# Performance work log

Hardware: AMD Instinct MI355X
Metric: run time of the kernel (lower is better)

The kernel has to match this reference:

```python
import jax, jax.numpy as jnp
import numpy as np

N = 100000          # nodes
E = 1600000         # edges (before self-loops)
F_IN = 512          # num_node_features
H1, C1 = 8, 8       # layer-1 heads, per-head channels
NUM_CLASSES = 40
NEG_SLOPE = 0.2     # PyG GATConv default


def setup_inputs() -> dict:
    key = jax.random.key(0)
    ks = jax.random.split(key, 10)
    x = jax.random.normal(ks[0], (N, F_IN), jnp.float32)
    edge_index = jax.random.randint(ks[1], (2, E), 0, N, dtype=jnp.int64)
    # Glorot-ish scaled params (matches PyG init scale qualitatively)
    W1 = jax.random.normal(ks[2], (F_IN, H1 * C1), jnp.float32) / np.sqrt(F_IN)
    a_src1 = jax.random.normal(ks[3], (H1, C1), jnp.float32) / np.sqrt(C1)
    a_dst1 = jax.random.normal(ks[4], (H1, C1), jnp.float32) / np.sqrt(C1)
    b1 = jnp.zeros((H1 * C1,), jnp.float32)
    W2 = jax.random.normal(ks[5], (H1 * C1, NUM_CLASSES), jnp.float32) / np.sqrt(H1 * C1)
    a_src2 = jax.random.normal(ks[6], (1, NUM_CLASSES), jnp.float32) / np.sqrt(NUM_CLASSES)
    a_dst2 = jax.random.normal(ks[7], (1, NUM_CLASSES), jnp.float32) / np.sqrt(NUM_CLASSES)
    b2 = jnp.zeros((NUM_CLASSES,), jnp.float32)
    return {"x": x, "edge_index": edge_index, "W1": W1, "a_src1": a_src1,
            "a_dst1": a_dst1, "b1": b1, "W2": W2, "a_src2": a_src2,
            "a_dst2": a_dst2, "b2": b2}


def gat_layer(x, src, dst, W, a_s, a_d, b, concat):
    """PyG GATConv (eval mode: dropout=0). src -> dst messages, softmax over dst."""
    heads, ch = a_s.shape
    n = x.shape[0]
    h = (x @ W).reshape(n, heads, ch)                      # [N,H,C]
    alpha_s = jnp.einsum('nhc,hc->nh', h, a_s)             # [N,H]
    alpha_d = jnp.einsum('nhc,hc->nh', h, a_d)
    e = jax.nn.leaky_relu(alpha_s[src] + alpha_d[dst], NEG_SLOPE)   # [E,H]
    # segment softmax over incoming edges of each dst node
    m = jax.ops.segment_max(e, dst, num_segments=n)        # [N,H]
    p = jnp.exp(e - m[dst])
    s = jax.ops.segment_sum(p, dst, num_segments=n)
    alpha = p / (s[dst] + 1e-16)                           # [E,H]
    out = jax.ops.segment_sum(h[src] * alpha[..., None], dst, num_segments=n)  # [N,H,C]
    out = out.reshape(n, heads * ch) if concat else out.mean(axis=1)
    return out + b


def reference(x, edge_index, W1, a_src1, a_dst1, b1, W2, a_src2, a_dst2, b2):
    n = x.shape[0]
    loops = jnp.arange(n, dtype=edge_index.dtype)
    src = jnp.concatenate([edge_index[0], loops])          # add self-loops (PyG default)
    dst = jnp.concatenate([edge_index[1], loops])
    h = gat_layer(x, src, dst, W1, a_src1, a_dst1, b1, concat=True)
    h = jax.nn.elu(h)
    out = gat_layer(h, src, dst, W2, a_src2, a_dst2, b2, concat=False)
    return jax.nn.log_softmax(out, axis=1)
```

## Files before the change

kernel.cpp:

```cpp
#include <hip/hip_runtime.h>
#include <hip/hip_bf16.h>
#include <hip/hip_fp16.h>

#define F_IN 512
#define HC1 64
#define NH1 8
#define NC 40
#define NEG_SLOPE 0.2f
#define SCAN_CHUNK 2048
#define RADIX_EPB 4096
#define MAXNB 512
#define BCAP 8192

typedef short bf16x8 __attribute__((ext_vector_type(8)));
typedef float f32x4 __attribute__((ext_vector_type(4)));

static __device__ __forceinline__ unsigned short f2b(float f) {
    __hip_bfloat16 h = __float2bfloat16(f);
    return *(unsigned short*)&h;
}
static __device__ __forceinline__ float b2f(unsigned short u) {
    union { unsigned int i; float f; } v;
    v.i = ((unsigned int)u) << 16;
    return v.f;
}
static __device__ __forceinline__ unsigned short f2h(float f) {
    __half h = __float2half(f);
    return *(unsigned short*)&h;
}

__global__ void detect_i64(const int* __restrict__ ei, int* __restrict__ flag, int n_check) {
    __shared__ int found;
    if (threadIdx.x == 0) found = 0;
    __syncthreads();
    for (int i = threadIdx.x; i < n_check; i += 256) {
        if (ei[2 * i + 1] != 0) atomicOr(&found, 1);
    }
    __syncthreads();
    if (threadIdx.x == 0) *flag = (found == 0) ? 1 : 0;
}

__global__ void prep(const float* __restrict__ W1, const float* __restrict__ W2,
                     const float* __restrict__ a_s2, const float* __restrict__ a_d2,
                     unsigned short* __restrict__ wst, float* __restrict__ ws2,
                     float* __restrict__ wd2) {
    int t = blockIdx.x * 256 + threadIdx.x;
    if (t < 4096) {
        int p  = t & 7;
        int n  = (t >> 3) & 63;
        int kb = t >> 9;
        int l  = p ^ (n & 7);
        int k0 = kb * 64 + l * 8;
        unsigned short v[8];
#pragma unroll
        for (int j = 0; j < 8; j++) v[j] = f2b(W1[(size_t)(k0 + j) * HC1 + n]);
        *(uint4*)(wst + ((size_t)(kb * 64 + n) * 64 + p * 8)) = *(uint4*)v;
    }
    if (blockIdx.x == 0 && threadIdx.x < HC1) {
        int c = threadIdx.x;
        float s = 0.f, d = 0.f;
#pragma unroll
        for (int j = 0; j < NC; j++) {
            float w = W2[c * NC + j];
            s += w * a_s2[j];
            d += w * a_d2[j];
        }
        ws2[c] = s;
        wd2[c] = d;
    }
}

__global__ __launch_bounds__(256) void scatter1(const int* __restrict__ ei, const int* __restrict__ flag,
                                                int* __restrict__ deg, int* __restrict__ bcnt,
                                                int2* __restrict__ bpairs, int E, int NB) {
    __shared__ int cnt[MAXNB];
    __shared__ int gb[MAXNB];
    int tid = threadIdx.x;
    for (int i = tid; i < NB; i += 256) cnt[i] = 0;
    __syncthreads();
    int f = *flag;
    int base = blockIdx.x * RADIX_EPB;
    int sv[16], dv[16], rv[16];
#pragma unroll
    for (int i = 0; i < 16; i++) {
        int e = base + i * 256 + tid;
        if (e < E) {
            int s, d;
            if (f) { s = ei[2 * e]; d = ei[2 * (E + e)]; }
            else   { s = ei[e];     d = ei[E + e]; }
            sv[i] = s; dv[i] = d;
            rv[i] = atomicAdd(&cnt[d >> 8], 1);
            atomicAdd(&deg[d], 1);
        }
    }
    __syncthreads();
    for (int i = tid; i < NB; i += 256) {
        int c = cnt[i];
        gb[i] = c ? atomicAdd(&bcnt[i], c) : 0;
    }
    __syncthreads();
#pragma unroll
    for (int i = 0; i < 16; i++) {
        int e = base + i * 256 + tid;
        if (e < E) {
            int pos = gb[dv[i] >> 8] + rv[i];
            if (pos < BCAP)
                bpairs[(size_t)(dv[i] >> 8) * BCAP + pos] = make_int2(sv[i], dv[i]);
        }
    }
}

__global__ __launch_bounds__(256) void scan1(const int* __restrict__ deg, int* __restrict__ rowptr,
                                             int* __restrict__ bsums, int n) {
    __shared__ int sbuf[256];
    int tid = threadIdx.x;
    int base = blockIdx.x * SCAN_CHUNK + tid * 8;
    int v[8];
#pragma unroll
    for (int j = 0; j < 8; j++) { int idx = base + j; v[j] = (idx < n) ? deg[idx] : 0; }
    int tsum = 0;
#pragma unroll
    for (int j = 0; j < 8; j++) tsum += v[j];
    sbuf[tid] = tsum;
    __syncthreads();
    for (int off = 1; off < 256; off <<= 1) {
        int t = (tid >= off) ? sbuf[tid - off] : 0;
        __syncthreads();
        sbuf[tid] += t;
        __syncthreads();
    }
    int run = sbuf[tid] - tsum;
#pragma unroll
    for (int j = 0; j < 8; j++) {
        run += v[j];
        int idx = base + j;
        if (idx < n) rowptr[1 + idx] = run;
    }
    if (tid == 255) bsums[blockIdx.x] = sbuf[255];
}

__global__ __launch_bounds__(256) void scan23(int* __restrict__ rowptr,
                                              const int* __restrict__ bsums, int n, int nb) {
    __shared__ int soff[64];
    int tid = threadIdx.x;
    if (tid < 64) {
        int lane = tid;
        int v = (lane < nb) ? bsums[lane] : 0;
        int orig = v;
        for (int off = 1; off < 64; off <<= 1) {
            int t = __shfl_up(v, (unsigned)off, 64);
            if (lane >= off) v += t;
        }
        soff[lane] = v - orig;
    }
    __syncthreads();
    int i = blockIdx.x * 256 + tid;
    if (i < n) {
        rowptr[1 + i] += soff[i >> 11];
        if (i == 0) rowptr[0] = 0;
    }
}

__global__ __launch_bounds__(256) void scatter2(const int2* __restrict__ bpairs,
                                                const int* __restrict__ bcnt,
                                                const int* __restrict__ rowptr,
                                                int* __restrict__ col, int Nn) {
    __shared__ int cur[256];
    int b = blockIdx.x;
    int node0 = b << 8;
    int tid = threadIdx.x;
    int nlast = min(node0 + 256, Nn);
    if (node0 + tid < nlast) cur[tid] = rowptr[node0 + tid];
    __syncthreads();
    int cnt = min(bcnt[b], BCAP);
    const int2* bp = bpairs + (size_t)b * BCAP;
    for (int j = tid; j < cnt; j += 256) {
        int2 pr = bp[j];
        int pos = atomicAdd(&cur[pr.y - node0], 1);
        col[pos] = pr.x;
    }
}

__global__ __launch_bounds__(256) void gemm1(const float* __restrict__ x,
                                             const unsigned short* __restrict__ wst,
                                             const float* __restrict__ a_s, const float* __restrict__ a_d,
                                             unsigned short* __restrict__ h1, float* __restrict__ as1,
                                             float* __restrict__ ad1, int Nn) {
    __shared__ __align__(16) unsigned short smem[8192];
    unsigned short* xs = smem;
    unsigned short* ws = smem + 4096;
    int tid = threadIdx.x;
    int m0 = blockIdx.x * 64;
    int w = tid >> 6, lane = tid & 63;
    int quad = lane >> 4, mr = lane & 15;
    f32x4 acc[4];
#pragma unroll
    for (int i = 0; i < 4; i++) acc[i] = (f32x4){0.f, 0.f, 0.f, 0.f};

    int srow = tid >> 2;
    int sseg = tid & 3;
    bool rok = (m0 + srow) < Nn;
    const float* xrow = x + (size_t)(m0 + srow) * F_IN + sseg * 16;
    int swzw = (srow & 7) << 4;
    int swzr = (mr & 7) << 4;

    for (int kb = 0; kb < 8; kb++) {
        float4 xv0, xv1, xv2, xv3;
        if (rok) {
            const float4* xp = (const float4*)(xrow + kb * 64);
            xv0 = xp[0]; xv1 = xp[1]; xv2 = xp[2]; xv3 = xp[3];
        } else {
            xv0 = xv1 = xv2 = xv3 = make_float4(0.f, 0.f, 0.f, 0.f);
        }
        const uint4* wp = (const uint4*)(wst + (size_t)kb * 4096);
        uint4 wv0 = wp[tid];
        uint4 wv1 = wp[tid + 256];
        __syncthreads();
        {
            unsigned short bx[16];
            bx[0]  = f2b(xv0.x); bx[1]  = f2b(xv0.y); bx[2]  = f2b(xv0.z); bx[3]  = f2b(xv0.w);
            bx[4]  = f2b(xv1.x); bx[5]  = f2b(xv1.y); bx[6]  = f2b(xv1.z); bx[7]  = f2b(xv1.w);
            bx[8]  = f2b(xv2.x); bx[9]  = f2b(xv2.y); bx[10] = f2b(xv2.z); bx[11] = f2b(xv2.w);
            bx[12] = f2b(xv3.x); bx[13] = f2b(xv3.y); bx[14] = f2b(xv3.z); bx[15] = f2b(xv3.w);
            unsigned short* xr = xs + srow * 64;
            *(uint4*)(xr + ((((sseg * 32)      ) ^ swzw) >> 1)) = *(uint4*)&bx[0];
            *(uint4*)(xr + ((((sseg * 32) + 16 ) ^ swzw) >> 1)) = *(uint4*)&bx[8];
            ((uint4*)ws)[tid]       = wv0;
            ((uint4*)ws)[tid + 256] = wv1;
        }
        __syncthreads();
#pragma unroll
        for (int ks = 0; ks < 2; ks++) {
            int kc = ks * 64 + quad * 16;
            int co = (kc ^ swzr) >> 1;
            bf16x8 a = *(const bf16x8*)(xs + (w * 16 + mr) * 64 + co);
#pragma unroll
            for (int nb = 0; nb < 4; nb++) {
                bf16x8 b = *(const bf16x8*)(ws + (nb * 16 + mr) * 64 + co);
                acc[nb] = __builtin_amdgcn_mfma_f32_16x16x32_bf16(a, b, acc[nb], 0, 0, 0);
            }
        }
    }
    __syncthreads();
    unsigned short (*hs)[72] = (unsigned short(*)[72])smem;
#pragma unroll
    for (int nb = 0; nb < 4; nb++)
#pragma unroll
        for (int r = 0; r < 4; r++)
            hs[w * 16 + quad * 4 + r][nb * 16 + mr] = f2b(acc[nb][r]);
    __syncthreads();
    {
        if (rok) {
            uint4 v0 = *(const uint4*)&hs[srow][sseg * 16];
            uint4 v1 = *(const uint4*)&hs[srow][sseg * 16 + 8];
            uint4* dst = (uint4*)(h1 + (size_t)(m0 + srow) * HC1 + sseg * 16);
            dst[0] = v0;
            dst[1] = v1;
        }
    }
    for (int i = tid; i < 512; i += 256) {
        int row = i >> 3, hh = i & 7;
        if (m0 + row < Nn) {
            float s = 0.f, d = 0.f;
#pragma unroll
            for (int c = 0; c < 8; c++) {
                float v = b2f(hs[row][hh * 8 + c]);
                s += v * a_s[hh * 8 + c];
                d += v * a_d[hh * 8 + c];
            }
            as1[(size_t)(m0 + row) * NH1 + hh] = s;
            ad1[(size_t)(m0 + row) * NH1 + hh] = d;
        }
    }
}

__device__ __forceinline__ float lrelu(float e) { return e > 0.f ? e : NEG_SLOPE * e; }

__global__ __launch_bounds__(256) void agg1(const unsigned short* __restrict__ h1,
                                            const float* __restrict__ as1,
                                            const float* __restrict__ ad1, const int* __restrict__ rowptr,
                                            const int* __restrict__ col, const float* __restrict__ b1,
                                            const float* __restrict__ ws2, const float* __restrict__ wd2,
                                            unsigned short* __restrict__ h2b, float* __restrict__ as2,
                                            float* __restrict__ ad2, int Nn) {
    __shared__ float pbuf[4][NH1 * 68];
    int w = threadIdx.x >> 6;
    int wave = (blockIdx.x * 256 + threadIdx.x) >> 6;
    int lane = threadIdx.x & 63;
    if (wave >= Nn) return;
    int d = wave;
    int jb = rowptr[d], je = rowptr[d + 1];
    int half = lane >> 5;
    int cl = lane & 31;
    int head = cl >> 2;
    const float4* as4 = (const float4*)as1;
    const float4* ad4 = (const float4*)ad1;

    float4 dd0 = ad4[d * 2], dd1 = ad4[d * 2 + 1];
    float adh[8] = {dd0.x, dd0.y, dd0.z, dd0.w, dd1.x, dd1.y, dd1.z, dd1.w};
    float4 sd0 = as4[d * 2], sd1 = as4[d * 2 + 1];
    float svh[8] = {sd0.x, sd0.y, sd0.z, sd0.w, sd1.x, sd1.y, sd1.z, sd1.w};
    float e0[8];
#pragma unroll
    for (int h = 0; h < NH1; h++) e0[h] = lrelu(svh[h] + adh[h]);

    float acc0, acc1, ss;
    {
        unsigned gv = *(const unsigned*)(h1 + (size_t)d * HC1 + 2 * cl);
        union { unsigned i; float f; } lo, hi;
        lo.i = gv << 16; hi.i = gv & 0xffff0000u;
        if (half == 0) { acc0 = lo.f; acc1 = hi.f; ss = 1.f; }
        else           { acc0 = 0.f;  acc1 = 0.f;  ss = 0.f; }
    }
    float* pb = pbuf[w];

    for (int c0 = jb; c0 < je; c0 += 64) {
        int nc = min(64, je - c0);
        int srcv = d;
        if (lane < nc) {
            unsigned u = (unsigned)col[c0 + lane];
            srcv = (u < (unsigned)Nn) ? (int)u : d;
            float4 a0 = as4[srcv * 2], a1 = as4[srcv * 2 + 1];
            float ev[8] = {a0.x, a0.y, a0.z, a0.w, a1.x, a1.y, a1.z, a1.w};
#pragma unroll
            for (int h = 0; h < NH1; h++)
                pb[h * 68 + lane] = __expf(lrelu(ev[h] + adh[h]) - e0[h]);
        } else {
#pragma unroll
            for (int h = 0; h < NH1; h++) pb[h * 68 + lane] = 0.f;
        }
        int ncp = (nc + 7) & ~7;
        for (int jj = 0; jj < ncp; jj += 8) {
#pragma unroll
            for (int u4 = 0; u4 < 4; u4++) {
                int idx = jj + 2 * u4 + half;
                int s = __shfl(srcv, idx, 64);
                float p = pb[head * 68 + idx];
                unsigned gv = *(const unsigned*)(h1 + (size_t)s * HC1 + 2 * cl);
                union { unsigned i; float f; } lo, hi;
                lo.i = gv << 16; hi.i = gv & 0xffff0000u;
                acc0 += p * lo.f;
                acc1 += p * hi.f;
                ss += p;
            }
        }
    }
    acc0 += __shfl_xor(acc0, 32, 64);
    acc1 += __shfl_xor(acc1, 32, 64);
    ss   += __shfl_xor(ss, 32, 64);
    float inv = 1.f / (ss + 1e-16f);
    float o0 = acc0 * inv + b1[2 * cl];
    float o1 = acc1 * inv + b1[2 * cl + 1];
    o0 = o0 > 0.f ? o0 : __expf(o0) - 1.0f;
    o1 = o1 > 0.f ? o1 : __expf(o1) - 1.0f;
    if (half == 0) {
        unsigned pk = (unsigned)f2h(o0) | ((unsigned)f2h(o1) << 16);
        *(unsigned*)(h2b + (size_t)d * HC1 + 2 * cl) = pk;
    }
    float va = o0 * ws2[2 * cl] + o1 * ws2[2 * cl + 1];
    float vd = o0 * wd2[2 * cl] + o1 * wd2[2 * cl + 1];
#pragma unroll
    for (int off = 16; off; off >>= 1) {
        va += __shfl_xor(va, off, 64);
        vd += __shfl_xor(vd, off, 64);
    }
    if (lane == 0) { as2[d] = va; ad2[d] = vd; }
}

__global__ __launch_bounds__(256) void agg2(const unsigned short* __restrict__ h2b,
                                            const float* __restrict__ as2,
                                            const float* __restrict__ ad2, const int* __restrict__ rowptr,
                                            const int* __restrict__ col, const float* __restrict__ W2,
                                            const float* __restrict__ b2,
                                            float* __restrict__ out, int Nn) {
    __shared__ float pbuf[4][64];
    __shared__ float smv[4][64];
    __shared__ float W2s[HC1 * NC];
    int tid = threadIdx.x;
    for (int i = tid; i < HC1 * NC; i += 256) W2s[i] = W2[i];
    __syncthreads();
    int w = tid >> 6;
    int wave = (blockIdx.x * 256 + tid) >> 6;
    int lane = tid & 63;
    if (wave >= Nn) return;
    int d = wave;
    int jb = rowptr[d], je = rowptr[d + 1];
    int half = lane >> 5;
    int cl = lane & 31;
    float adv = ad2[d];
    float e0 = lrelu(as2[d] + adv);
    float acc0, acc1, ss;
    {
        unsigned gv = *(const unsigned*)(h2b + (size_t)d * HC1 + 2 * cl);
        union { unsigned u; __half2 h; } cv; cv.u = gv;
        float2 ff = __half22float2(cv.h);
        if (half == 0) { acc0 = ff.x; acc1 = ff.y; ss = 1.f; }
        else           { acc0 = 0.f;  acc1 = 0.f;  ss = 0.f; }
    }
    float* pb = pbuf[w];

    for (int c0 = jb; c0 < je; c0 += 64) {
        int nc = min(64, je - c0);
        int srcv = d;
        if (lane < nc) {
            unsigned u = (unsigned)col[c0 + lane];
            srcv = (u < (unsigned)Nn) ? (int)u : d;
            pb[lane] = __expf(lrelu(as2[srcv] + adv) - e0);
        } else {
            pb[lane] = 0.f;
        }
        int ncp = (nc + 7) & ~7;
        for (int jj = 0; jj < ncp; jj += 8) {
#pragma unroll
            for (int u4 = 0; u4 < 4; u4++) {
                int idx = jj + 2 * u4 + half;
                int s = __shfl(srcv, idx, 64);
                float p = pb[idx];
                unsigned gv = *(const unsigned*)(h2b + (size_t)s * HC1 + 2 * cl);
                union { unsigned u; __half2 h; } cv; cv.u = gv;
                float2 ff = __half22float2(cv.h);
                acc0 += p * ff.x;
                acc1 += p * ff.y;
                ss += p;
            }
        }
    }
    acc0 += __shfl_xor(acc0, 32, 64);
    acc1 += __shfl_xor(acc1, 32, 64);
    ss   += __shfl_xor(ss, 32, 64);
    float inv = 1.f / (ss + 1e-16f);
    if (half == 0) {
        smv[w][2 * cl]     = acc0 * inv;
        smv[w][2 * cl + 1] = acc1 * inv;
    }
    float o = 0.f;
    if (lane < NC) {
        o = b2[lane];
        const float* sv = smv[w];
#pragma unroll
        for (int c = 0; c < HC1; c++) o += sv[c] * W2s[c * NC + lane];
    }
    float vm = (lane < NC) ? o : -1e30f;
#pragma unroll
    for (int off = 32; off; off >>= 1) vm = fmaxf(vm, __shfl_xor(vm, off, 64));
    float ex = (lane < NC) ? __expf(o - vm) : 0.f;
#pragma unroll
    for (int off = 32; off; off >>= 1) ex += __shfl_xor(ex, off, 64);
    float lsm = o - vm - __logf(ex);
    if (lane < NC) out[(size_t)d * NC + lane] = lsm;
}

extern "C" void kernel_launch(void* const* d_in, const int* in_sizes, int n_in,
                              void* d_out, int out_size, void* d_ws, size_t ws_size,
                              hipStream_t stream) {
    const float* x      = (const float*)d_in[0];
    const int*   ei     = (const int*)d_in[1];
    const float* W1     = (const float*)d_in[2];
    const float* a_src1 = (const float*)d_in[3];
    const float* a_dst1 = (const float*)d_in[4];
    const float* b1     = (const float*)d_in[5];
    const float* W2     = (const float*)d_in[6];
    const float* a_src2 = (const float*)d_in[7];
    const float* a_dst2 = (const float*)d_in[8];
    const float* b2     = (const float*)d_in[9];
    float* out = (float*)d_out;

    const int N = in_sizes[0] / F_IN;
    const int E = in_sizes[1] / 2;
    const int NB = (N + 255) >> 8;

    char* p = (char*)d_ws;
    auto alloc = [&](size_t bytes) -> void* {
        void* r = (void*)p;
        p += (bytes + 255) & ~(size_t)255;
        return r;
    };
    int* deg    = (int*)alloc((size_t)N * 4);
    int* bcnt   = (int*)alloc((size_t)MAXNB * 4);
    int* rowptr = (int*)alloc(((size_t)N + 1) * 4);
    int* bsums  = (int*)alloc(64 * 4);
    int* flag   = (int*)alloc(256);
    int2* bpairs = (int2*)alloc((size_t)NB * BCAP * 8);
    int* col    = (int*)alloc((size_t)E * 4);
    unsigned short* h1  = (unsigned short*)alloc((size_t)N * HC1 * 2);
    float* as1  = (float*)alloc((size_t)N * NH1 * 4);
    float* ad1  = (float*)alloc((size_t)N * NH1 * 4);
    unsigned short* h2b = (unsigned short*)alloc((size_t)N * HC1 * 2);
    float* as2  = (float*)alloc((size_t)N * 4);
    float* ad2  = (float*)alloc((size_t)N * 4);
    unsigned short* wst = (unsigned short*)alloc(8 * 64 * 64 * 2);
    float* ws2  = (float*)alloc(HC1 * 4);
    float* wd2  = (float*)alloc(HC1 * 4);

    size_t zlen = (size_t)((char*)(bcnt + MAXNB) - (char*)deg);
    hipMemsetAsync(deg, 0, zlen, stream);
    detect_i64<<<1, 256, 0, stream>>>(ei, flag, 4096);
    prep<<<16, 256, 0, stream>>>(W1, W2, a_src2, a_dst2, wst, ws2, wd2);
    scatter1<<<(E + RADIX_EPB - 1) / RADIX_EPB, 256, 0, stream>>>(ei, flag, deg, bcnt, bpairs, E, NB);
    int nb = (N + SCAN_CHUNK - 1) / SCAN_CHUNK;
    scan1<<<nb, 256, 0, stream>>>(deg, rowptr, bsums, N);
    scan23<<<(N + 255) / 256, 256, 0, stream>>>(rowptr, bsums, N, nb);
    scatter2<<<NB, 256, 0, stream>>>(bpairs, bcnt, rowptr, col, N);

    gemm1<<<(N + 63) / 64, 256, 0, stream>>>(x, wst, a_src1, a_dst1, h1, as1, ad1, N);
    agg1<<<(N + 3) / 4, 256, 0, stream>>>(h1, as1, ad1, rowptr, col, b1, ws2, wd2, h2b, as2, ad2, N);

    agg2<<<(N + 3) / 4, 256, 0, stream>>>(h2b, as2, ad2, rowptr, col, W2, b2, out, N);
}
```

Measured before the change: 584.5 us.

## Widen per-lane gathers in GAT aggregation and fold int64 detection into prep

In agg1, each lane now gathers 4 bf16 channels (8-byte loads) and 4 neighbours are processed concurrently per wave instead of 2. In agg2, each lane gathers 8 fp16 channels (16-byte loads) and 8 neighbours run in parallel. The aim is fewer, wider memory transactions and more edges in flight per wave, paid for with extra cross-lane shuffle reductions and more accumulator registers. Separately, the int64 detection kernel is merged into prep as an extra block, removing one kernel launch.

```diff
diff --git a/kernel.cpp b/kernel.cpp
--- a/kernel.cpp
+++ b/kernel.cpp
@@ -29,23 +29,24 @@
     return *(unsigned short*)&h;
 }
 
-__global__ void detect_i64(const int* __restrict__ ei, int* __restrict__ flag, int n_check) {
-    __shared__ int found;
-    if (threadIdx.x == 0) found = 0;
-    __syncthreads();
-    for (int i = threadIdx.x; i < n_check; i += 256) {
-        if (ei[2 * i + 1] != 0) atomicOr(&found, 1);
-    }
-    __syncthreads();
-    if (threadIdx.x == 0) *flag = (found == 0) ? 1 : 0;
-}
-
 __global__ void prep(const float* __restrict__ W1, const float* __restrict__ W2,
                      const float* __restrict__ a_s2, const float* __restrict__ a_d2,
+                     const int* __restrict__ ei,
                      unsigned short* __restrict__ wst, float* __restrict__ ws2,
-                     float* __restrict__ wd2) {
+                     float* __restrict__ wd2, int* __restrict__ flag) {
+    if (blockIdx.x == 16) {
+        __shared__ int found;
+        if (threadIdx.x == 0) found = 0;
+        __syncthreads();
+        for (int i = threadIdx.x; i < 4096; i += 256) {
+            if (ei[2 * i + 1] != 0) atomicOr(&found, 1);
+        }
+        __syncthreads();
+        if (threadIdx.x == 0) *flag = (found == 0) ? 1 : 0;
+        return;
+    }
     int t = blockIdx.x * 256 + threadIdx.x;
-    if (t < 4096) {
+    {
         int p  = t & 7;
         int n  = (t >> 3) & 63;
         int kb = t >> 9;
@@ -290,9 +291,9 @@
     if (wave >= Nn) return;
     int d = wave;
     int jb = rowptr[d], je = rowptr[d + 1];
-    int half = lane >> 5;
-    int cl = lane & 31;
-    int head = cl >> 2;
+    int g = lane >> 4;
+    int cl = lane & 15;
+    int head = cl >> 1;
     const float4* as4 = (const float4*)as1;
     const float4* ad4 = (const float4*)ad1;
 
@@ -304,13 +305,13 @@
 #pragma unroll
     for (int h = 0; h < NH1; h++) e0[h] = lrelu(svh[h] + adh[h]);
 
-    float acc0, acc1, ss;
-    {
-        unsigned gv = *(const unsigned*)(h1 + (size_t)d * HC1 + 2 * cl);
-        union { unsigned i; float f; } lo, hi;
-        lo.i = gv << 16; hi.i = gv & 0xffff0000u;
-        if (half == 0) { acc0 = lo.f; acc1 = hi.f; ss = 1.f; }
-        else           { acc0 = 0.f;  acc1 = 0.f;  ss = 0.f; }
+    float a0 = 0.f, a1 = 0.f, a2 = 0.f, a3 = 0.f, ss = 0.f;
+    if (g == 0) {
+        uint2 gv = *(const uint2*)(h1 + (size_t)d * HC1 + 4 * cl);
+        union { unsigned i; float f; } t0, t1, t2, t3;
+        t0.i = gv.x << 16; t1.i = gv.x & 0xffff0000u;
+        t2.i = gv.y << 16; t3.i = gv.y & 0xffff0000u;
+        a0 = t0.f; a1 = t1.f; a2 = t2.f; a3 = t3.f; ss = 1.f;
     }
     float* pb = pbuf[w];
 
@@ -320,8 +321,8 @@
         if (lane < nc) {
             unsigned u = (unsigned)col[c0 + lane];
             srcv = (u < (unsigned)Nn) ? (int)u : d;
-            float4 a0 = as4[srcv * 2], a1 = as4[srcv * 2 + 1];
-            float ev[8] = {a0.x, a0.y, a0.z, a0.w, a1.x, a1.y, a1.z, a1.w};
+            float4 q0 = as4[srcv * 2], q1 = as4[srcv * 2 + 1];
+            float ev[8] = {q0.x, q0.y, q0.z, q0.w, q1.x, q1.y, q1.z, q1.w};
 #pragma unroll
             for (int h = 0; h < NH1; h++)
                 pb[h * 68 + lane] = __expf(lrelu(ev[h] + adh[h]) - e0[h]);
@@ -332,35 +333,50 @@
         int ncp = (nc + 7) & ~7;
         for (int jj = 0; jj < ncp; jj += 8) {
 #pragma unroll
-            for (int u4 = 0; u4 < 4; u4++) {
-                int idx = jj + 2 * u4 + half;
+            for (int u2 = 0; u2 < 2; u2++) {
+                int idx = jj + 4 * u2 + g;
                 int s = __shfl(srcv, idx, 64);
                 float p = pb[head * 68 + idx];
-                unsigned gv = *(const unsigned*)(h1 + (size_t)s * HC1 + 2 * cl);
-                union { unsigned i; float f; } lo, hi;
-                lo.i = gv << 16; hi.i = gv & 0xffff0000u;
-                acc0 += p * lo.f;
-                acc1 += p * hi.f;
+                uint2 gv = *(const uint2*)(h1 + (size_t)s * HC1 + 4 * cl);
+                union { unsigned i; float f; } t0, t1, t2, t3;
+                t0.i = gv.x << 16; t1.i = gv.x & 0xffff0000u;
+                t2.i = gv.y << 16; t3.i = gv.y & 0xffff0000u;
+                a0 += p * t0.f; a1 += p * t1.f;
+                a2 += p * t2.f; a3 += p * t3.f;
                 ss += p;
             }
         }
     }
-    acc0 += __shfl_xor(acc0, 32, 64);
-    acc1 += __shfl_xor(acc1, 32, 64);
-    ss   += __shfl_xor(ss, 32, 64);
+#pragma unroll
+    for (int off = 16; off <= 32; off <<= 1) {
+        a0 += __shfl_xor(a0, off, 64);
+        a1 += __shfl_xor(a1, off, 64);
+        a2 += __shfl_xor(a2, off, 64);
+        a3 += __shfl_xor(a3, off, 64);
+        ss += __shfl_xor(ss, off, 64);
+    }
     float inv = 1.f / (ss + 1e-16f);
-    float o0 = acc0 * inv + b1[2 * cl];
-    float o1 = acc1 * inv + b1[2 * cl + 1];
+    float4 bv = *(const float4*)(b1 + 4 * cl);
+    float o0 = a0 * inv + bv.x;
+    float o1 = a1 * inv + bv.y;
+    float o2 = a2 * inv + bv.z;
+    float o3 = a3 * inv + bv.w;
     o0 = o0 > 0.f ? o0 : __expf(o0) - 1.0f;
     o1 = o1 > 0.f ? o1 : __expf(o1) - 1.0f;
-    if (half == 0) {
-        unsigned pk = (unsigned)f2h(o0) | ((unsigned)f2h(o1) << 16);
-        *(unsigned*)(h2b + (size_t)d * HC1 + 2 * cl) = pk;
-    }
-    float va = o0 * ws2[2 * cl] + o1 * ws2[2 * cl + 1];
-    float vd = o0 * wd2[2 * cl] + o1 * wd2[2 * cl + 1];
-#pragma unroll
-    for (int off = 16; off; off >>= 1) {
+    o2 = o2 > 0.f ? o2 : __expf(o2) - 1.0f;
+    o3 = o3 > 0.f ? o3 : __expf(o3) - 1.0f;
+    if (g == 0) {
+        uint2 pk;
+        pk.x = (unsigned)f2h(o0) | ((unsigned)f2h(o1) << 16);
+        pk.y = (unsigned)f2h(o2) | ((unsigned)f2h(o3) << 16);
+        *(uint2*)(h2b + (size_t)d * HC1 + 4 * cl) = pk;
+    }
+    float4 wsv = *(const float4*)(ws2 + 4 * cl);
+    float4 wdv = *(const float4*)(wd2 + 4 * cl);
+    float va = o0 * wsv.x + o1 * wsv.y + o2 * wsv.z + o3 * wsv.w;
+    float vd = o0 * wdv.x + o1 * wdv.y + o2 * wdv.z + o3 * wdv.w;
+#pragma unroll
+    for (int off = 1; off <= 8; off <<= 1) {
         va += __shfl_xor(va, off, 64);
         vd += __shfl_xor(vd, off, 64);
     }
@@ -385,17 +401,24 @@
     if (wave >= Nn) return;
     int d = wave;
     int jb = rowptr[d], je = rowptr[d + 1];
-    int half = lane >> 5;
-    int cl = lane & 31;
+    int g = lane >> 3;
+    int cl = lane & 7;
     float adv = ad2[d];
     float e0 = lrelu(as2[d] + adv);
-    float acc0, acc1, ss;
-    {
-        unsigned gv = *(const unsigned*)(h2b + (size_t)d * HC1 + 2 * cl);
-        union { unsigned u; __half2 h; } cv; cv.u = gv;
-        float2 ff = __half22float2(cv.h);
-        if (half == 0) { acc0 = ff.x; acc1 = ff.y; ss = 1.f; }
-        else           { acc0 = 0.f;  acc1 = 0.f;  ss = 0.f; }
+    float ac[8];
+    float ss = 0.f;
+#pragma unroll
+    for (int i = 0; i < 8; i++) ac[i] = 0.f;
+    if (g == 0) {
+        uint4 gv = *(const uint4*)(h2b + (size_t)d * HC1 + 8 * cl);
+        const unsigned* gw = (const unsigned*)&gv;
+#pragma unroll
+        for (int j = 0; j < 4; j++) {
+            union { unsigned u; __half2 h; } cv; cv.u = gw[j];
+            float2 ff = __half22float2(cv.h);
+            ac[2 * j] = ff.x; ac[2 * j + 1] = ff.y;
+        }
+        ss = 1.f;
     }
     float* pb = pbuf[w];
 
@@ -409,29 +432,38 @@
         } else {
             pb[lane] = 0.f;
         }
-        int ncp = (nc + 7) & ~7;
-        for (int jj = 0; jj < ncp; jj += 8) {
-#pragma unroll
-            for (int u4 = 0; u4 < 4; u4++) {
-                int idx = jj + 2 * u4 + half;
+        int ncp = (nc + 15) & ~15;
+        for (int jj = 0; jj < ncp; jj += 16) {
+#pragma unroll
+            for (int u2 = 0; u2 < 2; u2++) {
+                int idx = jj + 8 * u2 + g;
                 int s = __shfl(srcv, idx, 64);
                 float p = pb[idx];
-                unsigned gv = *(const unsigned*)(h2b + (size_t)s * HC1 + 2 * cl);
-                union { unsigned u; __half2 h; } cv; cv.u = gv;
-                float2 ff = __half22float2(cv.h);
-                acc0 += p * ff.x;
-                acc1 += p * ff.y;
+                uint4 gv = *(const uint4*)(h2b + (size_t)s * HC1 + 8 * cl);
+                const unsigned* gw = (const unsigned*)&gv;
+#pragma unroll
+                for (int j = 0; j < 4; j++) {
+                    union { unsigned u; __half2 h; } cv; cv.u = gw[j];
+                    float2 ff = __half22float2(cv.h);
+                    ac[2 * j]     += p * ff.x;
+                    ac[2 * j + 1] += p * ff.y;
+                }
                 ss += p;
             }
         }
     }
-    acc0 += __shfl_xor(acc0, 32, 64);
-    acc1 += __shfl_xor(acc1, 32, 64);
-    ss   += __shfl_xor(ss, 32, 64);
+#pragma unroll
+    for (int off = 8; off <= 32; off <<= 1) {
+#pragma unroll
+        for (int i = 0; i < 8; i++) ac[i] += __shfl_xor(ac[i], off, 64);
+        ss += __shfl_xor(ss, off, 64);
+    }
     float inv = 1.f / (ss + 1e-16f);
-    if (half == 0) {
-        smv[w][2 * cl]     = acc0 * inv;
-        smv[w][2 * cl + 1] = acc1 * inv;
+    if (g == 0) {
+        float4 v0 = make_float4(ac[0] * inv, ac[1] * inv, ac[2] * inv, ac[3] * inv);
+        float4 v1 = make_float4(ac[4] * inv, ac[5] * inv, ac[6] * inv, ac[7] * inv);
+        *(float4*)&smv[w][8 * cl]     = v0;
+        *(float4*)&smv[w][8 * cl + 4] = v1;
     }
     float o = 0.f;
     if (lane < NC) {
@@ -494,8 +526,7 @@
 
     size_t zlen = (size_t)((char*)(bcnt + MAXNB) - (char*)deg);
     hipMemsetAsync(deg, 0, zlen, stream);
-    detect_i64<<<1, 256, 0, stream>>>(ei, flag, 4096);
-    prep<<<16, 256, 0, stream>>>(W1, W2, a_src2, a_dst2, wst, ws2, wd2);
+    prep<<<17, 256, 0, stream>>>(W1, W2, a_src2, a_dst2, ei, wst, ws2, wd2, flag);
     scatter1<<<(E + RADIX_EPB - 1) / RADIX_EPB, 256, 0, stream>>>(ei, flag, deg, bcnt, bpairs, E, NB);
     int nb = (N + SCAN_CHUNK - 1) / SCAN_CHUNK;
     scan1<<<nb, 256, 0, stream>>>(deg, rowptr, bsums, N);
```

After: 588.0 us. Within noise of the previous version (+0.6%).

## Replace CSR build with 64-node edge buckets and shared-memory atomic aggregation

Applied to the files above, without the earlier changes.

Drops the degree count, prefix scans and second scatter pass. Edges are bucketed by destination into blocks of 64 nodes, stored as packed (src<<6 | local dst) ints, and each block accumulates messages into LDS with atomics. The i64 detection is folded into the prep launch. This saves several launches and CSR passes, but it adds LDS atomic contention, silently drops edges when a bucket exceeds its fixed capacity, and relies on src fitting in 25 bits.

```diff
diff --git a/kernel.cpp b/kernel.cpp
--- a/kernel.cpp
+++ b/kernel.cpp
@@ -7,10 +7,9 @@
 #define NH1 8
 #define NC 40
 #define NEG_SLOPE 0.2f
-#define SCAN_CHUNK 2048
 #define RADIX_EPB 4096
-#define MAXNB 512
-#define BCAP 8192
+#define MAXNB2 2048
+#define BCAP2 2048
 
 typedef short bf16x8 __attribute__((ext_vector_type(8)));
 typedef float f32x4 __attribute__((ext_vector_type(4)));
@@ -29,23 +28,26 @@
     return *(unsigned short*)&h;
 }
 
-__global__ void detect_i64(const int* __restrict__ ei, int* __restrict__ flag, int n_check) {
-    __shared__ int found;
-    if (threadIdx.x == 0) found = 0;
-    __syncthreads();
-    for (int i = threadIdx.x; i < n_check; i += 256) {
-        if (ei[2 * i + 1] != 0) atomicOr(&found, 1);
-    }
-    __syncthreads();
-    if (threadIdx.x == 0) *flag = (found == 0) ? 1 : 0;
-}
+__device__ __forceinline__ float lrelu(float e) { return e > 0.f ? e : NEG_SLOPE * e; }
 
 __global__ void prep(const float* __restrict__ W1, const float* __restrict__ W2,
                      const float* __restrict__ a_s2, const float* __restrict__ a_d2,
+                     const int* __restrict__ ei,
                      unsigned short* __restrict__ wst, float* __restrict__ ws2,
-                     float* __restrict__ wd2) {
+                     float* __restrict__ wd2, int* __restrict__ flag) {
+    if (blockIdx.x == 16) {
+        __shared__ int found;
+        if (threadIdx.x == 0) found = 0;
+        __syncthreads();
+        for (int i = threadIdx.x; i < 4096; i += 256) {
+            if (ei[2 * i + 1] != 0) atomicOr(&found, 1);
+        }
+        __syncthreads();
+        if (threadIdx.x == 0) *flag = (found == 0) ? 1 : 0;
+        return;
+    }
     int t = blockIdx.x * 256 + threadIdx.x;
-    if (t < 4096) {
+    {
         int p  = t & 7;
         int n  = (t >> 3) & 63;
         int kb = t >> 9;
@@ -71,16 +73,16 @@
 }
 
 __global__ __launch_bounds__(256) void scatter1(const int* __restrict__ ei, const int* __restrict__ flag,
-                                                int* __restrict__ deg, int* __restrict__ bcnt,
-                                                int2* __restrict__ bpairs, int E, int NB) {
-    __shared__ int cnt[MAXNB];
-    __shared__ int gb[MAXNB];
+                                                int* __restrict__ bcnt, int* __restrict__ bpk,
+                                                int E, int NB2) {
+    __shared__ int cnt[MAXNB2];
+    __shared__ int gb[MAXNB2];
     int tid = threadIdx.x;
-    for (int i = tid; i < NB; i += 256) cnt[i] = 0;
+    for (int i = tid; i < NB2; i += 256) cnt[i] = 0;
     __syncthreads();
     int f = *flag;
     int base = blockIdx.x * RADIX_EPB;
-    int sv[16], dv[16], rv[16];
+    int pk[16], bk[16], rv[16];
 #pragma unroll
     for (int i = 0; i < 16; i++) {
         int e = base + i * 256 + tid;
@@ -88,13 +90,13 @@
             int s, d;
             if (f) { s = ei[2 * e]; d = ei[2 * (E + e)]; }
             else   { s = ei[e];     d = ei[E + e]; }
-            sv[i] = s; dv[i] = d;
-            rv[i] = atomicAdd(&cnt[d >> 8], 1);
-            atomicAdd(&deg[d], 1);
-        }
-    }
-    __syncthreads();
-    for (int i = tid; i < NB; i += 256) {
+            pk[i] = (s << 6) | (d & 63);
+            bk[i] = d >> 6;
+            rv[i] = atomicAdd(&cnt[bk[i]], 1);
+        }
+    }
+    __syncthreads();
+    for (int i = tid; i < NB2; i += 256) {
         int c = cnt[i];
         gb[i] = c ? atomicAdd(&bcnt[i], c) : 0;
     }
@@ -103,81 +105,10 @@
     for (int i = 0; i < 16; i++) {
         int e = base + i * 256 + tid;
         if (e < E) {
-            int pos = gb[dv[i] >> 8] + rv[i];
-            if (pos < BCAP)
-                bpairs[(size_t)(dv[i] >> 8) * BCAP + pos] = make_int2(sv[i], dv[i]);
-        }
-    }
-}
-
-__global__ __launch_bounds__(256) void scan1(const int* __restrict__ deg, int* __restrict__ rowptr,
-                                             int* __restrict__ bsums, int n) {
-    __shared__ int sbuf[256];
-    int tid = threadIdx.x;
-    int base = blockIdx.x * SCAN_CHUNK + tid * 8;
-    int v[8];
-#pragma unroll
-    for (int j = 0; j < 8; j++) { int idx = base + j; v[j] = (idx < n) ? deg[idx] : 0; }
-    int tsum = 0;
-#pragma unroll
-    for (int j = 0; j < 8; j++) tsum += v[j];
-    sbuf[tid] = tsum;
-    __syncthreads();
-    for (int off = 1; off < 256; off <<= 1) {
-        int t = (tid >= off) ? sbuf[tid - off] : 0;
-        __syncthreads();
-        sbuf[tid] += t;
-        __syncthreads();
-    }
-    int run = sbuf[tid] - tsum;
-#pragma unroll
-    for (int j = 0; j < 8; j++) {
-        run += v[j];
-        int idx = base + j;
-        if (idx < n) rowptr[1 + idx] = run;
-    }
-    if (tid == 255) bsums[blockIdx.x] = sbuf[255];
-}
-
-__global__ __launch_bounds__(256) void scan23(int* __restrict__ rowptr,
-                                              const int* __restrict__ bsums, int n, int nb) {
-    __shared__ int soff[64];
-    int tid = threadIdx.x;
-    if (tid < 64) {
-        int lane = tid;
-        int v = (lane < nb) ? bsums[lane] : 0;
-        int orig = v;
-        for (int off = 1; off < 64; off <<= 1) {
-            int t = __shfl_up(v, (unsigned)off, 64);
-            if (lane >= off) v += t;
-        }
-        soff[lane] = v - orig;
-    }
-    __syncthreads();
-    int i = blockIdx.x * 256 + tid;
-    if (i < n) {
-        rowptr[1 + i] += soff[i >> 11];
-        if (i == 0) rowptr[0] = 0;
-    }
-}
-
-__global__ __launch_bounds__(256) void scatter2(const int2* __restrict__ bpairs,
-                                                const int* __restrict__ bcnt,
-                                                const int* __restrict__ rowptr,
-                                                int* __restrict__ col, int Nn) {
-    __shared__ int cur[256];
-    int b = blockIdx.x;
-    int node0 = b << 8;
-    int tid = threadIdx.x;
-    int nlast = min(node0 + 256, Nn);
-    if (node0 + tid < nlast) cur[tid] = rowptr[node0 + tid];
-    __syncthreads();
-    int cnt = min(bcnt[b], BCAP);
-    const int2* bp = bpairs + (size_t)b * BCAP;
-    for (int j = tid; j < cnt; j += 256) {
-        int2 pr = bp[j];
-        int pos = atomicAdd(&cur[pr.y - node0], 1);
-        col[pos] = pr.x;
+            int pos = gb[bk[i]] + rv[i];
+            if (pos < BCAP2)
+                bpk[(size_t)bk[i] * BCAP2 + pos] = pk[i];
+        }
     }
 }
 
@@ -274,180 +205,217 @@
     }
 }
 
-__device__ __forceinline__ float lrelu(float e) { return e > 0.f ? e : NEG_SLOPE * e; }
-
-__global__ __launch_bounds__(256) void agg1(const unsigned short* __restrict__ h1,
-                                            const float* __restrict__ as1,
-                                            const float* __restrict__ ad1, const int* __restrict__ rowptr,
-                                            const int* __restrict__ col, const float* __restrict__ b1,
-                                            const float* __restrict__ ws2, const float* __restrict__ wd2,
-                                            unsigned short* __restrict__ h2b, float* __restrict__ as2,
-                                            float* __restrict__ ad2, int Nn) {
-    __shared__ float pbuf[4][NH1 * 68];
-    int w = threadIdx.x >> 6;
-    int wave = (blockIdx.x * 256 + threadIdx.x) >> 6;
-    int lane = threadIdx.x & 63;
-    if (wave >= Nn) return;
-    int d = wave;
-    int jb = rowptr[d], je = rowptr[d + 1];
-    int half = lane >> 5;
-    int cl = lane & 31;
-    int head = cl >> 2;
-    const float4* as4 = (const float4*)as1;
-    const float4* ad4 = (const float4*)ad1;
-
-    float4 dd0 = ad4[d * 2], dd1 = ad4[d * 2 + 1];
-    float adh[8] = {dd0.x, dd0.y, dd0.z, dd0.w, dd1.x, dd1.y, dd1.z, dd1.w};
-    float4 sd0 = as4[d * 2], sd1 = as4[d * 2 + 1];
-    float svh[8] = {sd0.x, sd0.y, sd0.z, sd0.w, sd1.x, sd1.y, sd1.z, sd1.w};
-    float e0[8];
-#pragma unroll
-    for (int h = 0; h < NH1; h++) e0[h] = lrelu(svh[h] + adh[h]);
-
-    float acc0, acc1, ss;
+__global__ __launch_bounds__(256) void agg1b(const unsigned short* __restrict__ h1,
+                                             const float* __restrict__ as1,
+                                             const float* __restrict__ ad1,
+                                             const int* __restrict__ bcnt, const int* __restrict__ bpk,
+                                             const float* __restrict__ b1,
+                                             const float* __restrict__ ws2, const float* __restrict__ wd2,
+                                             unsigned short* __restrict__ h2b, float* __restrict__ as2,
+                                             float* __restrict__ ad2, int Nn) {
+    __shared__ float acc[64][68];
+    __shared__ float psum1[64][8];
+    __shared__ float ad1s[64][8];
+    __shared__ float e0s[64][8];
+    int tid = threadIdx.x;
+    int b = blockIdx.x;
+    int node0 = b << 6;
     {
-        unsigned gv = *(const unsigned*)(h1 + (size_t)d * HC1 + 2 * cl);
-        union { unsigned i; float f; } lo, hi;
-        lo.i = gv << 16; hi.i = gv & 0xffff0000u;
-        if (half == 0) { acc0 = lo.f; acc1 = hi.f; ss = 1.f; }
-        else           { acc0 = 0.f;  acc1 = 0.f;  ss = 0.f; }
-    }
-    float* pb = pbuf[w];
-
-    for (int c0 = jb; c0 < je; c0 += 64) {
-        int nc = min(64, je - c0);
-        int srcv = d;
-        if (lane < nc) {
-            unsigned u = (unsigned)col[c0 + lane];
-            srcv = (u < (unsigned)Nn) ? (int)u : d;
-            float4 a0 = as4[srcv * 2], a1 = as4[srcv * 2 + 1];
-            float ev[8] = {a0.x, a0.y, a0.z, a0.w, a1.x, a1.y, a1.z, a1.w};
-#pragma unroll
-            for (int h = 0; h < NH1; h++)
-                pb[h * 68 + lane] = __expf(lrelu(ev[h] + adh[h]) - e0[h]);
-        } else {
-#pragma unroll
-            for (int h = 0; h < NH1; h++) pb[h * 68 + lane] = 0.f;
-        }
-        int ncp = (nc + 7) & ~7;
-        for (int jj = 0; jj < ncp; jj += 8) {
-#pragma unroll
-            for (int u4 = 0; u4 < 4; u4++) {
-                int idx = jj + 2 * u4 + half;
-                int s = __shfl(srcv, idx, 64);
-                float p = pb[head * 68 + idx];
-                unsigned gv = *(const unsigned*)(h1 + (size_t)s * HC1 + 2 * cl);
-                union { unsigned i; float f; } lo, hi;
-                lo.i = gv << 16; hi.i = gv & 0xffff0000u;
-                acc0 += p * lo.f;
-                acc1 += p * hi.f;
-                ss += p;
-            }
-        }
-    }
-    acc0 += __shfl_xor(acc0, 32, 64);
-    acc1 += __shfl_xor(acc1, 32, 64);
-    ss   += __shfl_xor(ss, 32, 64);
-    float inv = 1.f / (ss + 1e-16f);
-    float o0 = acc0 * inv + b1[2 * cl];
-    float o1 = acc1 * inv + b1[2 * cl + 1];
-    o0 = o0 > 0.f ? o0 : __expf(o0) - 1.0f;
-    o1 = o1 > 0.f ? o1 : __expf(o1) - 1.0f;
-    if (half == 0) {
-        unsigned pk = (unsigned)f2h(o0) | ((unsigned)f2h(o1) << 16);
-        *(unsigned*)(h2b + (size_t)d * HC1 + 2 * cl) = pk;
-    }
-    float va = o0 * ws2[2 * cl] + o1 * ws2[2 * cl + 1];
-    float vd = o0 * wd2[2 * cl] + o1 * wd2[2 * cl + 1];
-#pragma unroll
-    for (int off = 16; off; off >>= 1) {
-        va += __shfl_xor(va, off, 64);
-        vd += __shfl_xor(vd, off, 64);
-    }
-    if (lane == 0) { as2[d] = va; ad2[d] = vd; }
-}
-
-__global__ __launch_bounds__(256) void agg2(const unsigned short* __restrict__ h2b,
-                                            const float* __restrict__ as2,
-                                            const float* __restrict__ ad2, const int* __restrict__ rowptr,
-                                            const int* __restrict__ col, const float* __restrict__ W2,
-                                            const float* __restrict__ b2,
-                                            float* __restrict__ out, int Nn) {
-    __shared__ float pbuf[4][64];
-    __shared__ float smv[4][64];
+        int n = tid >> 3, seg = tid & 7;
+#pragma unroll
+        for (int pass = 0; pass < 2; pass++) {
+            int nn = pass * 32 + n;
+            int gn = node0 + nn;
+            uint4 hv = make_uint4(0, 0, 0, 0);
+            if (gn < Nn) hv = *(const uint4*)(h1 + (size_t)gn * HC1 + seg * 8);
+            const unsigned* hw = (const unsigned*)&hv;
+#pragma unroll
+            for (int j = 0; j < 4; j++) {
+                acc[nn][seg * 8 + 2 * j]     = b2f((unsigned short)(hw[j] & 0xffff));
+                acc[nn][seg * 8 + 2 * j + 1] = b2f((unsigned short)(hw[j] >> 16));
+            }
+        }
+    }
+    for (int i = tid; i < 512; i += 256) {
+        int n = i >> 3, h = i & 7;
+        int gn = node0 + n;
+        float adv = 0.f, asv = 0.f;
+        if (gn < Nn) { adv = ad1[(size_t)gn * 8 + h]; asv = as1[(size_t)gn * 8 + h]; }
+        ad1s[n][h] = adv;
+        e0s[n][h] = lrelu(asv + adv);
+        psum1[n][h] = 1.f;
+    }
+    __syncthreads();
+    int cb = min(bcnt[b], BCAP2);
+    const int* bp = bpk + (size_t)b * BCAP2;
+    int w = tid >> 6, lane = tid & 63;
+    int g = lane >> 3, cl = lane & 7;
+    for (int eb = w * 16; eb < cb; eb += 64) {
+        int eA = eb + g, eB = eb + 8 + g;
+        int pkA = (eA < cb) ? bp[eA] : -1;
+        int pkB = (eB < cb) ? bp[eB] : -1;
+        if (pkA >= 0) {
+            int src = pkA >> 6, dl = pkA & 63;
+            float p = __expf(lrelu(as1[(size_t)src * 8 + cl] + ad1s[dl][cl]) - e0s[dl][cl]);
+            uint4 hv = *(const uint4*)(h1 + (size_t)src * HC1 + cl * 8);
+            const unsigned* hw = (const unsigned*)&hv;
+#pragma unroll
+            for (int j = 0; j < 4; j++) {
+                atomicAdd(&acc[dl][cl * 8 + 2 * j],     p * b2f((unsigned short)(hw[j] & 0xffff)));
+                atomicAdd(&acc[dl][cl * 8 + 2 * j + 1], p * b2f((unsigned short)(hw[j] >> 16)));
+            }
+            atomicAdd(&psum1[dl][cl], p);
+        }
+        if (pkB >= 0) {
+            int src = pkB >> 6, dl = pkB & 63;
+            float p = __expf(lrelu(as1[(size_t)src * 8 + cl] + ad1s[dl][cl]) - e0s[dl][cl]);
+            uint4 hv = *(const uint4*)(h1 + (size_t)src * HC1 + cl * 8);
+            const unsigned* hw = (const unsigned*)&hv;
+#pragma unroll
+            for (int j = 0; j < 4; j++) {
+                atomicAdd(&acc[dl][cl * 8 + 2 * j],     p * b2f((unsigned short)(hw[j] & 0xffff)));
+                atomicAdd(&acc[dl][cl * 8 + 2 * j + 1], p * b2f((unsigned short)(hw[j] >> 16)));
+            }
+            atomicAdd(&psum1[dl][cl], p);
+        }
+    }
+    __syncthreads();
+    {
+        int nloc = tid >> 5;
+        int c2 = (tid & 31) * 2;
+        int hh = c2 >> 3;
+        float2 bv = *(const float2*)(b1 + c2);
+        float2 wsv = *(const float2*)(ws2 + c2);
+        float2 wdv = *(const float2*)(wd2 + c2);
+#pragma unroll
+        for (int pass = 0; pass < 8; pass++) {
+            int n = pass * 8 + nloc;
+            int gn = node0 + n;
+            if (gn < Nn) {
+                float inv = 1.f / (psum1[n][hh] + 1e-16f);
+                float o0 = acc[n][c2] * inv + bv.x;
+                float o1 = acc[n][c2 + 1] * inv + bv.y;
+                o0 = o0 > 0.f ? o0 : __expf(o0) - 1.0f;
+                o1 = o1 > 0.f ? o1 : __expf(o1) - 1.0f;
+                unsigned pk = (unsigned)f2h(o0) | ((unsigned)f2h(o1) << 16);
+                *(unsigned*)(h2b + (size_t)gn * HC1 + c2) = pk;
+                float va = o0 * wsv.x + o1 * wsv.y;
+                float vd = o0 * wdv.x + o1 * wdv.y;
+#pragma unroll
+                for (int off = 1; off <= 16; off <<= 1) {
+                    va += __shfl_xor(va, off, 64);
+                    vd += __shfl_xor(vd, off, 64);
+                }
+                if ((tid & 31) == 0) { as2[gn] = va; ad2[gn] = vd; }
+            }
+        }
+    }
+}
+
+__global__ __launch_bounds__(256) void agg2b(const unsigned short* __restrict__ h2b,
+                                             const float* __restrict__ as2,
+                                             const float* __restrict__ ad2,
+                                             const int* __restrict__ bcnt, const int* __restrict__ bpk,
+                                             const float* __restrict__ W2, const float* __restrict__ b2,
+                                             float* __restrict__ out, int Nn) {
+    __shared__ float acc[64][68];
+    __shared__ float psum[64];
+    __shared__ float e0v[64], adv[64];
     __shared__ float W2s[HC1 * NC];
     int tid = threadIdx.x;
+    int b = blockIdx.x;
+    int node0 = b << 6;
     for (int i = tid; i < HC1 * NC; i += 256) W2s[i] = W2[i];
-    __syncthreads();
-    int w = tid >> 6;
-    int wave = (blockIdx.x * 256 + tid) >> 6;
-    int lane = tid & 63;
-    if (wave >= Nn) return;
-    int d = wave;
-    int jb = rowptr[d], je = rowptr[d + 1];
-    int half = lane >> 5;
-    int cl = lane & 31;
-    float adv = ad2[d];
-    float e0 = lrelu(as2[d] + adv);
-    float acc0, acc1, ss;
     {
-        unsigned gv = *(const unsigned*)(h2b + (size_t)d * HC1 + 2 * cl);
-        union { unsigned u; __half2 h; } cv; cv.u = gv;
-        float2 ff = __half22float2(cv.h);
-        if (half == 0) { acc0 = ff.x; acc1 = ff.y; ss = 1.f; }
-        else           { acc0 = 0.f;  acc1 = 0.f;  ss = 0.f; }
-    }
-    float* pb = pbuf[w];
-
-    for (int c0 = jb; c0 < je; c0 += 64) {
-        int nc = min(64, je - c0);
-        int srcv = d;
-        if (lane < nc) {
-            unsigned u = (unsigned)col[c0 + lane];
-            srcv = (u < (unsigned)Nn) ? (int)u : d;
-            pb[lane] = __expf(lrelu(as2[srcv] + adv) - e0);
-        } else {
-            pb[lane] = 0.f;
-        }
-        int ncp = (nc + 7) & ~7;
-        for (int jj = 0; jj < ncp; jj += 8) {
-#pragma unroll
-            for (int u4 = 0; u4 < 4; u4++) {
-                int idx = jj + 2 * u4 + half;
-                int s = __shfl(srcv, idx, 64);
-                float p = pb[idx];
-                unsigned gv = *(const unsigned*)(h2b + (size_t)s * HC1 + 2 * cl);
-                union { unsigned u; __half2 h; } cv; cv.u = gv;
+        int n = tid >> 3, seg = tid & 7;
+#pragma unroll
+        for (int pass = 0; pass < 2; pass++) {
+            int nn = pass * 32 + n;
+            int gn = node0 + nn;
+            uint4 hv = make_uint4(0, 0, 0, 0);
+            if (gn < Nn) hv = *(const uint4*)(h2b + (size_t)gn * HC1 + seg * 8);
+            const unsigned* hw = (const unsigned*)&hv;
+#pragma unroll
+            for (int j = 0; j < 4; j++) {
+                union { unsigned u; __half2 h; } cv; cv.u = hw[j];
                 float2 ff = __half22float2(cv.h);
-                acc0 += p * ff.x;
-                acc1 += p * ff.y;
-                ss += p;
-            }
-        }
-    }
-    acc0 += __shfl_xor(acc0, 32, 64);
-    acc1 += __shfl_xor(acc1, 32, 64);
-    ss   += __shfl_xor(ss, 32, 64);
-    float inv = 1.f / (ss + 1e-16f);
-    if (half == 0) {
-        smv[w][2 * cl]     = acc0 * inv;
-        smv[w][2 * cl + 1] = acc1 * inv;
-    }
-    float o = 0.f;
-    if (lane < NC) {
-        o = b2[lane];
-        const float* sv = smv[w];
-#pragma unroll
-        for (int c = 0; c < HC1; c++) o += sv[c] * W2s[c * NC + lane];
-    }
-    float vm = (lane < NC) ? o : -1e30f;
-#pragma unroll
-    for (int off = 32; off; off >>= 1) vm = fmaxf(vm, __shfl_xor(vm, off, 64));
-    float ex = (lane < NC) ? __expf(o - vm) : 0.f;
-#pragma unroll
-    for (int off = 32; off; off >>= 1) ex += __shfl_xor(ex, off, 64);
-    float lsm = o - vm - __logf(ex);
-    if (lane < NC) out[(size_t)d * NC + lane] = lsm;
+                acc[nn][seg * 8 + 2 * j]     = ff.x;
+                acc[nn][seg * 8 + 2 * j + 1] = ff.y;
+            }
+        }
+        if (tid < 64) {
+            psum[tid] = 1.f;
+            int gn = node0 + tid;
+            float a = 0.f, s = 0.f;
+            if (gn < Nn) { a = ad2[gn]; s = as2[gn]; }
+            adv[tid] = a;
+            e0v[tid] = lrelu(s + a);
+        }
+    }
+    __syncthreads();
+    int cb = min(bcnt[b], BCAP2);
+    const int* bp = bpk + (size_t)b * BCAP2;
+    int w = tid >> 6, lane = tid & 63;
+    int g = lane >> 3, cl = lane & 7;
+    for (int eb = w * 16; eb < cb; eb += 64) {
+        int eA = eb + g, eB = eb + 8 + g;
+        int pkA = (eA < cb) ? bp[eA] : -1;
+        int pkB = (eB < cb) ? bp[eB] : -1;
+        if (pkA >= 0) {
+            int src = pkA >> 6, dl = pkA & 63;
+            float p = __expf(lrelu(as2[src] + adv[dl]) - e0v[dl]);
+            uint4 hv = *(const uint4*)(h2b + (size_t)src * HC1 + cl * 8);
+            const unsigned* hw = (const unsigned*)&hv;
+#pragma unroll
+            for (int j = 0; j < 4; j++) {
+                union { unsigned u; __half2 h; } cv; cv.u = hw[j];
+                float2 ff = __half22float2(cv.h);
+                atomicAdd(&acc[dl][cl * 8 + 2 * j],     p * ff.x);
+                atomicAdd(&acc[dl][cl * 8 + 2 * j + 1], p * ff.y);
+            }
+            if (cl == 0) atomicAdd(&psum[dl], p);
+        }
+        if (pkB >= 0) {
+            int src = pkB >> 6, dl = pkB & 63;
+            float p = __expf(lrelu(as2[src] + adv[dl]) - e0v[dl]);
+            uint4 hv = *(const uint4*)(h2b + (size_t)src * HC1 + cl * 8);
+            const unsigned* hw = (const unsigned*)&hv;
+#pragma unroll
+            for (int j = 0; j < 4; j++) {
+                union { unsigned u; __half2 h; } cv; cv.u = hw[j];
+                float2 ff = __half22float2(cv.h);
+                atomicAdd(&acc[dl][cl * 8 + 2 * j],     p * ff.x);
+                atomicAdd(&acc[dl][cl * 8 + 2 * j + 1], p * ff.y);
+            }
+            if (cl == 0) atomicAdd(&psum[dl], p);
+        }
+    }
+    __syncthreads();
+    for (int i = 0; i < 16; i++) {
+        int n = w * 16 + i;
+        int gn = node0 + n;
+        if (gn >= Nn) break;
+        float inv = 1.f / (psum[n] + 1e-16f);
+        float o = 0.f;
+        if (lane < NC) {
+            float dot = 0.f;
+#pragma unroll
+            for (int c = 0; c < HC1; c += 4) {
+                float4 av = *(const float4*)&acc[n][c];
+                dot += av.x * W2s[(c + 0) * NC + lane] + av.y * W2s[(c + 1) * NC + lane]
+                     + av.z * W2s[(c + 2) * NC + lane] + av.w * W2s[(c + 3) * NC + lane];
+            }
+            o = b2[lane] + inv * dot;
+        }
+        float vm = (lane < NC) ? o : -1e30f;
+#pragma unroll
+        for (int off = 32; off; off >>= 1) vm = fmaxf(vm, __shfl_xor(vm, off, 64));
+        float ex = (lane < NC) ? __expf(o - vm) : 0.f;
+#pragma unroll
+        for (int off = 32; off; off >>= 1) ex += __shfl_xor(ex, off, 64);
+        float lsm = o - vm - __logf(ex);
+        if (lane < NC) out[(size_t)gn * NC + lane] = lsm;
+    }
 }
 
 extern "C" void kernel_launch(void* const* d_in, const int* in_sizes, int n_in,
@@ -467,7 +435,7 @@
 
     const int N = in_sizes[0] / F_IN;
     const int E = in_sizes[1] / 2;
-    const int NB = (N + 255) >> 8;
+    const int NB2 = (N + 63) >> 6;
 
     char* p = (char*)d_ws;
     auto alloc = [&](size_t bytes) -> void* {
@@ -475,13 +443,9 @@
         p += (bytes + 255) & ~(size_t)255;
         return r;
     };
-    int* deg    = (int*)alloc((size_t)N * 4);
-    int* bcnt   = (int*)alloc((size_t)MAXNB * 4);
-    int* rowptr = (int*)alloc(((size_t)N + 1) * 4);
-    int* bsums  = (int*)alloc(64 * 4);
+    int* bcnt   = (int*)alloc((size_t)NB2 * 4);
     int* flag   = (int*)alloc(256);
-    int2* bpairs = (int2*)alloc((size_t)NB * BCAP * 8);
-    int* col    = (int*)alloc((size_t)E * 4);
+    int* bpk    = (int*)alloc((size_t)NB2 * BCAP2 * 4);
     unsigned short* h1  = (unsigned short*)alloc((size_t)N * HC1 * 2);
     float* as1  = (float*)alloc((size_t)N * NH1 * 4);
     float* ad1  = (float*)alloc((size_t)N * NH1 * 4);
@@ -492,18 +456,12 @@
     float* ws2  = (float*)alloc(HC1 * 4);
     float* wd2  = (float*)alloc(HC1 * 4);
 
-    size_t zlen = (size_t)((char*)(bcnt + MAXNB) - (char*)deg);
-    hipMemsetAsync(deg, 0, zlen, stream);
-    detect_i64<<<1, 256, 0, stream>>>(ei, flag, 4096);
-    prep<<<16, 256, 0, stream>>>(W1, W2, a_src2, a_dst2, wst, ws2, wd2);
-    scatter1<<<(E + RADIX_EPB - 1) / RADIX_EPB, 256, 0, stream>>>(ei, flag, deg, bcnt, bpairs, E, NB);
-    int nb = (N + SCAN_CHUNK - 1) / SCAN_CHUNK;
-    scan1<<<nb, 256, 0, stream>>>(deg, rowptr, bsums, N);
-    scan23<<<(N + 255) / 256, 256, 0, stream>>>(rowptr, bsums, N, nb);
-    scatter2<<<NB, 256, 0, stream>>>(bpairs, bcnt, rowptr, col, N);
+    hipMemsetAsync(bcnt, 0, (size_t)NB2 * 4, stream);
+    prep<<<17, 256, 0, stream>>>(W1, W2, a_src2, a_dst2, ei, wst, ws2, wd2, flag);
+    scatter1<<<(E + RADIX_EPB - 1) / RADIX_EPB, 256, 0, stream>>>(ei, flag, bcnt, bpk, E, NB2);
 
     gemm1<<<(N + 63) / 64, 256, 0, stream>>>(x, wst, a_src1, a_dst1, h1, as1, ad1, N);
-    agg1<<<(N + 3) / 4, 256, 0, stream>>>(h1, as1, ad1, rowptr, col, b1, ws2, wd2, h2b, as2, ad2, N);
-
-    agg2<<<(N + 3) / 4, 256, 0, stream>>>(h2b, as2, ad2, rowptr, col, W2, b2, out, N);
-}
+    agg1b<<<NB2, 256, 0, stream>>>(h1, as1, ad1, bcnt, bpk, b1, ws2, wd2, h2b, as2, ad2, N);
+
+    agg2b<<<NB2, 256, 0, stream>>>(h2b, as2, ad2, bcnt, bpk, W2, b2, out, N);
+}
```

New measurement: 1.690 ms. 189% more time.
